# Optimization experiments

Measured on AMD Instinct MI355X. Metric: run time of the kernel, lower is better.

The kernel has to match this reference:

```python
import jax, jax.numpy as jnp
import numpy as np

B, N, C, H, D = 4, 2048, 1024, 16, 64
EPS = 1e-6

def setup_inputs() -> dict:
    key = jax.random.key(0)
    k1, k2, k3 = jax.random.split(key, 3)
    hidden_states = jax.random.normal(k1, (B, N, C), dtype=jnp.float32)
    qkv_w = jax.random.normal(k2, (3 * C, C), dtype=jnp.float32) * (C ** -0.5)
    out_w = jax.random.normal(k3, (C, C), dtype=jnp.float32) * (C ** -0.5)
    norm_q_w = jnp.ones((D,), dtype=jnp.float32)
    norm_k_w = jnp.ones((D,), dtype=jnp.float32)
    # RoPE tables: standard theta=10000 frequencies, rotate-half convention
    inv_freq = 1.0 / (10000.0 ** (jnp.arange(0, D, 2, dtype=jnp.float32) / D))
    pos = jnp.arange(N, dtype=jnp.float32)
    angles = pos[:, None] * inv_freq[None, :]              # [N, D/2]
    angles = jnp.concatenate([angles, angles], axis=-1)    # [N, D]
    cos = jnp.cos(angles)
    sin = jnp.sin(angles)
    return {"hidden_states": hidden_states, "cos": cos, "sin": sin,
            "qkv_w": qkv_w, "out_w": out_w,
            "norm_q_w": norm_q_w, "norm_k_w": norm_k_w}

def _rms_norm(x, w):
    # RMSNorm over last dim (head_dim)
    var = jnp.mean(jnp.square(x), axis=-1, keepdims=True)
    return x * jax.lax.rsqrt(var + EPS) * w

def _rotate_half(x):
    x1, x2 = jnp.split(x, 2, axis=-1)
    return jnp.concatenate([-x2, x1], axis=-1)

def reference(hidden_states, cos, sin, qkv_w, out_w, norm_q_w, norm_k_w):
    # fused QKV projection: [B,N,C] -> [B,N,3,H,D]
    qkv = jnp.einsum('bnc,oc->bno', hidden_states, qkv_w).reshape(B, N, 3, H, D)
    q, k, v = qkv[:, :, 0], qkv[:, :, 1], qkv[:, :, 2]   # each [B,N,H,D]
    q = _rms_norm(q, norm_q_w)
    k = _rms_norm(k, norm_k_w)
    # RoPE, broadcast cos/sin [N,D] -> [1,N,1,D]
    c = cos[None, :, None, :]
    s = sin[None, :, None, :]
    q = q * c + _rotate_half(q) * s
    k = k * c + _rotate_half(k) * s
    # SDPA: softmax(q k^T / sqrt(D)) v, no mask
    scale = D ** -0.5
    scores = jnp.einsum('bqhd,bkhd->bhqk', q, k) * scale   # [B,H,N,N]
    probs = jax.nn.softmax(scores, axis=-1)
    attn = jnp.einsum('bhqk,bkhd->bqhd', probs, v).reshape(B, N, C)
    return jnp.einsum('bnc,oc->bno', attn, out_w)
```

## Files before the change

### kernel.cpp

```cpp
#include <hip/hip_runtime.h>
#include <hip/hip_bf16.h>
#include <math.h>

typedef short bf16x8 __attribute__((ext_vector_type(8)));
typedef float f32x4 __attribute__((ext_vector_type(4)));
typedef float f32x16 __attribute__((ext_vector_type(16)));
typedef __hip_bfloat16 bf16;
typedef unsigned int uint;

static constexpr int Bn = 4, Nn = 2048, Cn = 1024, Hn = 16, Dn = 64;
static constexpr float kEps = 1e-6f;
static constexpr float kQScale = 0.125f * 1.44269504088896340f;

#define GLOAD_LDS16(gp, lp)                                                        \
  __builtin_amdgcn_global_load_lds(                                                \
      (const __attribute__((address_space(1))) unsigned int*)(gp),                 \
      (__attribute__((address_space(3))) unsigned int*)(lp), 16, 0, 0)

__device__ __forceinline__ float exp2_fast(float x) {
#if __has_builtin(__builtin_amdgcn_exp2f)
  return __builtin_amdgcn_exp2f(x);
#else
  return exp2f(x);
#endif
}

__global__ __launch_bounds__(256) void cvt_kernel(const float* __restrict__ in,
                                                  bf16* __restrict__ out, int n4) {
  int i = blockIdx.x * 256 + threadIdx.x;
  if (i >= n4) return;
  const float4 v = reinterpret_cast<const float4*>(in)[i];
  bf16 t[4];
  t[0] = __float2bfloat16(v.x); t[1] = __float2bfloat16(v.y);
  t[2] = __float2bfloat16(v.z); t[3] = __float2bfloat16(v.w);
  reinterpret_cast<uint2*>(out)[i] = *reinterpret_cast<const uint2*>(t);
}

template <int EPI>
__global__ __launch_bounds__(256) void gemm_bt(
    const bf16* __restrict__ A, const bf16* __restrict__ Bw,
    float* __restrict__ Cf, bf16* __restrict__ q_raw, bf16* __restrict__ k_raw,
    bf16* __restrict__ v_buf, const float* __restrict__ cosb,
    const float* __restrict__ sinb, const float* __restrict__ nqw,
    const float* __restrict__ nkw, int nxt, int nyt, int N, int K) {
  __shared__ __align__(16) bf16 As[2][128 * 64];
  __shared__ __align__(16) bf16 Bs[2][128 * 64];
  const int tid = threadIdx.x;
  const int lane = tid & 63, w = tid >> 6;
  const int wr = w >> 1, wc = w & 1;
  const int l15 = lane & 15, l4 = lane >> 4;
  const int bid = blockIdx.x;
  const int xcd = bid & 7;
  const int kk2 = bid >> 3;
  const int nslab = nxt >> 3;
  const int mtile = kk2 / nslab;
  const int ntile = xcd * nslab + (kk2 % nslab);
  const int m0 = mtile * 128, n0 = ntile * 128;
  f32x4 acc[4][4] = {};

  const int sr = tid >> 3, sc = (tid & 7) * 8;
  const int srcE = (((sc * 2) ^ ((sr & 7) << 4)) >> 1);
  const bf16* const Ap = A + (size_t)(m0 + sr) * K + srcE;
  const bf16* const Bp = Bw + (size_t)(n0 + sr) * K + srcE;

#pragma unroll
  for (int c = 0; c < 4; ++c) {
    GLOAD_LDS16(Ap + (size_t)(c * 32) * K, (char*)As[0] + tid * 16 + c * 4096);
    GLOAD_LDS16(Bp + (size_t)(c * 32) * K, (char*)Bs[0] + tid * 16 + c * 4096);
  }
  __syncthreads();

  const int swzg = (l15 & 7) << 4;
  int cur = 0;
  for (int k0 = 0; k0 < K; k0 += 64) {
    if (k0 + 64 < K) {
#pragma unroll
      for (int c = 0; c < 4; ++c) {
        GLOAD_LDS16(Ap + (size_t)(c * 32) * K + k0 + 64,
                    (char*)As[cur ^ 1] + tid * 16 + c * 4096);
        GLOAD_LDS16(Bp + (size_t)(c * 32) * K + k0 + 64,
                    (char*)Bs[cur ^ 1] + tid * 16 + c * 4096);
      }
    }
    const char* Ac = (const char*)As[cur];
    const char* Bc = (const char*)Bs[cur];
#pragma unroll
    for (int kc = 0; kc < 2; ++kc) {
      bf16x8 af[4], bfr[4];
#pragma unroll
      for (int mi = 0; mi < 4; ++mi)
        af[mi] = *reinterpret_cast<const bf16x8*>(
            Ac + (wr * 64 + mi * 16 + l15) * 128 + ((kc * 64 + l4 * 16) ^ swzg));
#pragma unroll
      for (int ni = 0; ni < 4; ++ni)
        bfr[ni] = *reinterpret_cast<const bf16x8*>(
            Bc + (wc * 64 + ni * 16 + l15) * 128 + ((kc * 64 + l4 * 16) ^ swzg));
#pragma unroll
      for (int mi = 0; mi < 4; ++mi)
#pragma unroll
        for (int ni = 0; ni < 4; ++ni)
          acc[mi][ni] =
              __builtin_amdgcn_mfma_f32_16x16x32_bf16(af[mi], bfr[ni], acc[mi][ni], 0, 0, 0);
    }
    __syncthreads();
    cur ^= 1;
  }

  if (EPI == 1) {
#pragma unroll
    for (int mi = 0; mi < 4; ++mi)
#pragma unroll
      for (int ni = 0; ni < 4; ++ni)
#pragma unroll
        for (int r = 0; r < 4; ++r) {
          const int row = m0 + wr * 64 + mi * 16 + l4 * 4 + r;
          const int col = n0 + wc * 64 + ni * 16 + l15;
          Cf[(size_t)row * N + col] = acc[mi][ni][r];
        }
    return;
  }

  const int colbase = n0 + wc * 64;
  const int which = colbase >> 10;
  const int hh = (colbase >> 6) & 15;
  if (which == 2) {
#pragma unroll
    for (int mi = 0; mi < 4; ++mi)
#pragma unroll
      for (int r = 0; r < 4; ++r) {
        const int row = m0 + wr * 64 + mi * 16 + l4 * 4 + r;
        const int b = row >> 11, n = row & (Nn - 1);
#pragma unroll
        for (int ni = 0; ni < 4; ++ni) {
          const int d = ni * 16 + l15;
          const size_t idx = (((size_t)b * Hn + hh) * Nn + n) * Dn + d;
          v_buf[idx] = __float2bfloat16(acc[mi][ni][r]);
        }
      }
    return;
  }
  const float* const wgt = which ? nkw : nqw;
  bf16* const dst = which ? k_raw : q_raw;
  float wv4[4];
#pragma unroll
  for (int ni = 0; ni < 4; ++ni) wv4[ni] = wgt[ni * 16 + l15];
#pragma unroll
  for (int mi = 0; mi < 4; ++mi)
#pragma unroll
    for (int r = 0; r < 4; ++r) {
      const int row = m0 + wr * 64 + mi * 16 + l4 * 4 + r;
      const int b = row >> 11, n = row & (Nn - 1);
      float x0 = acc[mi][0][r], x1 = acc[mi][1][r], x2 = acc[mi][2][r], x3 = acc[mi][3][r];
      float ss = x0 * x0 + x1 * x1 + x2 * x2 + x3 * x3;
      ss += __shfl_xor(ss, 1);
      ss += __shfl_xor(ss, 2);
      ss += __shfl_xor(ss, 4);
      ss += __shfl_xor(ss, 8);
      const float rinv = rsqrtf(ss * (1.f / Dn) + kEps);
      float nx[4] = {x0 * rinv * wv4[0], x1 * rinv * wv4[1], x2 * rinv * wv4[2],
                     x3 * rinv * wv4[3]};
#pragma unroll
      for (int ni = 0; ni < 4; ++ni) {
        const int d = ni * 16 + l15;
        const float c = cosb[n * Dn + d], s = sinb[n * Dn + d];
        const float sgn = (ni < 2) ? -1.f : 1.f;
        float val = nx[ni] * c + sgn * nx[ni ^ 2] * s;
        if (which == 0) val *= kQScale;
        const size_t idx = (((size_t)b * Hn + hh) * Nn + n) * Dn + d;
        dst[idx] = __float2bfloat16(val);
      }
    }
}

__global__ __launch_bounds__(256, 4) void flash_attn(
    const bf16* __restrict__ Qb, const bf16* __restrict__ Kb,
    const bf16* __restrict__ Vb, bf16* __restrict__ Ob) {
  __shared__ __align__(16) char KsB[2][32 * 128];
  __shared__ __align__(16) char VtB[2][64 * 64];
  const int bid = blockIdx.x;
  const int xcd = bid & 7;
  const int kidx = bid >> 3;
  const int bh = xcd * 8 + (kidx >> 4);
  const int q0 = (kidx & 15) * 128;
  const int tid = threadIdx.x, lane = tid & 63, w = tid >> 6;
  const int l31 = lane & 31, hi = lane >> 5;
  const bf16* Qp = Qb + (size_t)bh * Nn * Dn;
  const bf16* Kp = Kb + (size_t)bh * Nn * Dn;
  const bf16* Vp = Vb + (size_t)bh * Nn * Dn;

  const int qrow = q0 + w * 32 + l31;
  bf16x8 qf[4];
#pragma unroll
  for (int dm = 0; dm < 4; ++dm)
    qf[dm] = *reinterpret_cast<const bf16x8*>(&Qp[(size_t)qrow * Dn + dm * 16 + hi * 8]);

  f32x16 Ot0 = {}, Ot1 = {}, Lacc = {};

  const int skk = tid >> 3, sd0 = (tid & 7) * 8;
  const int srcKe = (((sd0 * 2) ^ ((skk & 7) << 4)) >> 1);

  auto stage_v = [&](char* Vn, const uint4& a) {
    const uint wa[4] = {a.x, a.y, a.z, a.w};
#pragma unroll
    for (int j = 0; j < 8; ++j) {
      const int d = sd0 + j;
      const int xs = (((d >> 1) ^ (d >> 3)) & 3) << 4;
      const unsigned short va = (j & 1) ? (unsigned short)(wa[j >> 1] >> 16)
                                        : (unsigned short)(wa[j >> 1] & 0xffff);
      *reinterpret_cast<unsigned short*>(Vn + d * 64 + ((skk * 2) ^ xs)) = va;
    }
  };

  GLOAD_LDS16(Kp + (size_t)skk * Dn + srcKe, KsB[0] + tid * 16);
  {
    uint4 cv = *reinterpret_cast<const uint4*>(&Vp[(size_t)skk * Dn + sd0]);
    stage_v(VtB[0], cv);
  }
  uint4 nv = *reinterpret_cast<const uint4*>(&Vp[(size_t)(32 + skk) * Dn + sd0]);
  __syncthreads();

  const int swzk_rd = (l31 & 7) << 4;
  const int xs0 = ((((l31) >> 1) ^ ((l31) >> 3)) & 3) << 4;
  const int xs1 = ((((32 + l31) >> 1) ^ ((32 + l31) >> 3)) & 3) << 4;
  int cur = 0;
  for (int k0 = 0; k0 < Nn; k0 += 32) {
    const char* Kc = KsB[cur];
    const char* Vc = VtB[cur];

    if (k0 + 32 < Nn) {
      GLOAD_LDS16(Kp + (size_t)(k0 + 32 + skk) * Dn + srcKe, KsB[cur ^ 1] + tid * 16);
      stage_v(VtB[cur ^ 1], nv);
      if (k0 + 64 < Nn)
        nv = *reinterpret_cast<const uint4*>(&Vp[(size_t)(k0 + 64 + skk) * Dn + sd0]);
    }

    f32x16 S0 = {};
    __builtin_amdgcn_s_setprio(1);
#pragma unroll
    for (int dm = 0; dm < 4; ++dm) {
      bf16x8 kf = *reinterpret_cast<const bf16x8*>(
          Kc + l31 * 128 + ((dm * 32 + hi * 16) ^ swzk_rd));
      S0 = __builtin_amdgcn_mfma_f32_32x32x16_bf16(kf, qf[dm], S0, 0, 0, 0);
    }
    __builtin_amdgcn_s_setprio(0);

#pragma unroll
    for (int i = 0; i < 16; ++i) S0[i] = exp2_fast(S0[i]);
#pragma unroll
    for (int i = 0; i < 16; ++i) Lacc[i] += S0[i];
    uint wv[8];
#pragma unroll
    for (int c = 0; c < 2; ++c) {
      uint w0, w1, w2, w3;
      asm("v_cvt_pk_bf16_f32 %0, %1, %2" : "=v"(w0) : "v"(S0[8 * c + 0]), "v"(S0[8 * c + 1]));
      asm("v_cvt_pk_bf16_f32 %0, %1, %2" : "=v"(w1) : "v"(S0[8 * c + 2]), "v"(S0[8 * c + 3]));
      asm("v_cvt_pk_bf16_f32 %0, %1, %2" : "=v"(w2) : "v"(S0[8 * c + 4]), "v"(S0[8 * c + 5]));
      asm("v_cvt_pk_bf16_f32 %0, %1, %2" : "=v"(w3) : "v"(S0[8 * c + 6]), "v"(S0[8 * c + 7]));
      asm("v_permlane32_swap_b32 %0, %1" : "+v"(w0), "+v"(w2));
      asm("v_permlane32_swap_b32 %0, %1" : "+v"(w1), "+v"(w3));
      wv[c * 4 + 0] = w0; wv[c * 4 + 1] = w1;
      wv[c * 4 + 2] = w2; wv[c * 4 + 3] = w3;
    }

    __builtin_amdgcn_s_setprio(1);
#pragma unroll
    for (int s = 0; s < 2; ++s) {
      const uint4 uu = {wv[s * 4 + 0], wv[s * 4 + 1], wv[s * 4 + 2], wv[s * 4 + 3]};
      const bf16x8 pa = __builtin_bit_cast(bf16x8, uu);
      bf16x8 vf0 = *reinterpret_cast<const bf16x8*>(
          Vc + l31 * 64 + ((s * 32 + hi * 16) ^ xs0));
      Ot0 = __builtin_amdgcn_mfma_f32_32x32x16_bf16(vf0, pa, Ot0, 0, 0, 0);
      bf16x8 vf1 = *reinterpret_cast<const bf16x8*>(
          Vc + (32 + l31) * 64 + ((s * 32 + hi * 16) ^ xs1));
      Ot1 = __builtin_amdgcn_mfma_f32_32x32x16_bf16(vf1, pa, Ot1, 0, 0, 0);
    }
    __builtin_amdgcn_s_setprio(0);

    __syncthreads();
    cur ^= 1;
  }

  float l_r = ((Lacc[0] + Lacc[1]) + (Lacc[2] + Lacc[3])) +
              ((Lacc[4] + Lacc[5]) + (Lacc[6] + Lacc[7])) +
              ((Lacc[8] + Lacc[9]) + (Lacc[10] + Lacc[11])) +
              ((Lacc[12] + Lacc[13]) + (Lacc[14] + Lacc[15]));
  l_r += __shfl_xor(l_r, 32);

  const float inv = 1.f / l_r;
  const int b = bh >> 4, h = bh & 15;
#pragma unroll
  for (int dc = 0; dc < 2; ++dc)
#pragma unroll
    for (int a2 = 0; a2 < 4; ++a2) {
      const f32x16& O = dc ? Ot1 : Ot0;
      unsigned short u0 = __bfloat16_as_ushort(__float2bfloat16(O[a2 * 4 + 0] * inv));
      unsigned short u1 = __bfloat16_as_ushort(__float2bfloat16(O[a2 * 4 + 1] * inv));
      unsigned short u2 = __bfloat16_as_ushort(__float2bfloat16(O[a2 * 4 + 2] * inv));
      unsigned short u3 = __bfloat16_as_ushort(__float2bfloat16(O[a2 * 4 + 3] * inv));
      uint2 pk;
      pk.x = (uint)u0 | ((uint)u1 << 16);
      pk.y = (uint)u2 | ((uint)u3 << 16);
      const int col = h * 64 + dc * 32 + a2 * 8 + hi * 4;
      *reinterpret_cast<uint2*>(&Ob[((size_t)(b * Nn + qrow)) * Cn + col]) = pk;
    }
}

extern "C" void kernel_launch(void* const* d_in, const int* in_sizes, int n_in,
                              void* d_out, int out_size, void* d_ws, size_t ws_size,
                              hipStream_t stream) {
  const float* hs   = (const float*)d_in[0];
  const float* cosb = (const float*)d_in[1];
  const float* sinb = (const float*)d_in[2];
  const float* qkvw = (const float*)d_in[3];
  const float* outw = (const float*)d_in[4];
  const float* nqw  = (const float*)d_in[5];
  const float* nkw  = (const float*)d_in[6];
  float* out = (float*)d_out;

  char* ws = (char*)d_ws;
  size_t off = 0;
  bf16* hs_b   = (bf16*)(ws + off); off += (size_t)Bn * Nn * Cn * 2;
  bf16* qkvw_b = (bf16*)(ws + off); off += (size_t)3 * Cn * Cn * 2;
  bf16* outw_b = (bf16*)(ws + off); off += (size_t)Cn * Cn * 2;
  bf16* q_raw  = (bf16*)(ws + off); off += (size_t)Bn * Hn * Nn * Dn * 2;
  bf16* k_raw  = (bf16*)(ws + off); off += (size_t)Bn * Hn * Nn * Dn * 2;
  bf16* v_buf  = (bf16*)(ws + off); off += (size_t)Bn * Hn * Nn * Dn * 2;
  bf16* attn   = (bf16*)(ws + off); off += (size_t)Bn * Nn * Cn * 2;

  cvt_kernel<<<(Bn * Nn * Cn / 4 + 255) / 256, 256, 0, stream>>>(hs, hs_b, Bn * Nn * Cn / 4);
  cvt_kernel<<<(3 * Cn * Cn / 4 + 255) / 256, 256, 0, stream>>>(qkvw, qkvw_b, 3 * Cn * Cn / 4);
  cvt_kernel<<<(Cn * Cn / 4 + 255) / 256, 256, 0, stream>>>(outw, outw_b, Cn * Cn / 4);

  gemm_bt<0><<<24 * 64, 256, 0, stream>>>(
      hs_b, qkvw_b, nullptr, q_raw, k_raw, v_buf, cosb, sinb, nqw, nkw,
      24, 64, 3 * Cn, Cn);

  flash_attn<<<Nn / 128 * Bn * Hn, 256, 0, stream>>>(q_raw, k_raw, v_buf, attn);

  gemm_bt<1><<<8 * 64, 256, 0, stream>>>(
      attn, outw_b, out, nullptr, nullptr, nullptr, nullptr, nullptr, nullptr, nullptr,
      8, 64, Cn, Cn);
}
```

Baseline: 202.9 us.

## Process two K/V tiles per barrier with four-slot LDS ring

The flash attention loop now stages two 32-key K/V tiles per iteration into a four-slot LDS ring and computes both before a single __syncthreads. This halves the number of block barriers and lets global loads for the next pair overlap with two tiles of compute. It doubles LDS use per block, to 32KB, and holds two prefetched V registers, which may reduce occupancy or raise register pressure.

```diff
diff --git a/kernel.cpp b/kernel.cpp
--- a/kernel.cpp
+++ b/kernel.cpp
@@ -175,8 +175,8 @@
 __global__ __launch_bounds__(256, 4) void flash_attn(
     const bf16* __restrict__ Qb, const bf16* __restrict__ Kb,
     const bf16* __restrict__ Vb, bf16* __restrict__ Ob) {
-  __shared__ __align__(16) char KsB[2][32 * 128];
-  __shared__ __align__(16) char VtB[2][64 * 64];
+  __shared__ __align__(16) char KsB[4][32 * 128];
+  __shared__ __align__(16) char VtB[4][64 * 64];
   const int bid = blockIdx.x;
   const int xcd = bid & 7;
   const int kidx = bid >> 3;
@@ -212,72 +212,84 @@
   };
 
   GLOAD_LDS16(Kp + (size_t)skk * Dn + srcKe, KsB[0] + tid * 16);
+  GLOAD_LDS16(Kp + (size_t)(32 + skk) * Dn + srcKe, KsB[1] + tid * 16);
   {
-    uint4 cv = *reinterpret_cast<const uint4*>(&Vp[(size_t)skk * Dn + sd0]);
-    stage_v(VtB[0], cv);
-  }
-  uint4 nv = *reinterpret_cast<const uint4*>(&Vp[(size_t)(32 + skk) * Dn + sd0]);
+    uint4 cv0 = *reinterpret_cast<const uint4*>(&Vp[(size_t)skk * Dn + sd0]);
+    uint4 cv1 = *reinterpret_cast<const uint4*>(&Vp[(size_t)(32 + skk) * Dn + sd0]);
+    stage_v(VtB[0], cv0);
+    stage_v(VtB[1], cv1);
+  }
+  uint4 nva = *reinterpret_cast<const uint4*>(&Vp[(size_t)(64 + skk) * Dn + sd0]);
+  uint4 nvb = *reinterpret_cast<const uint4*>(&Vp[(size_t)(96 + skk) * Dn + sd0]);
   __syncthreads();
 
   const int swzk_rd = (l31 & 7) << 4;
   const int xs0 = ((((l31) >> 1) ^ ((l31) >> 3)) & 3) << 4;
   const int xs1 = ((((32 + l31) >> 1) ^ ((32 + l31) >> 3)) & 3) << 4;
-  int cur = 0;
-  for (int k0 = 0; k0 < Nn; k0 += 32) {
-    const char* Kc = KsB[cur];
-    const char* Vc = VtB[cur];
-
-    if (k0 + 32 < Nn) {
-      GLOAD_LDS16(Kp + (size_t)(k0 + 32 + skk) * Dn + srcKe, KsB[cur ^ 1] + tid * 16);
-      stage_v(VtB[cur ^ 1], nv);
-      if (k0 + 64 < Nn)
-        nv = *reinterpret_cast<const uint4*>(&Vp[(size_t)(k0 + 64 + skk) * Dn + sd0]);
-    }
-
-    f32x16 S0 = {};
-    __builtin_amdgcn_s_setprio(1);
-#pragma unroll
-    for (int dm = 0; dm < 4; ++dm) {
-      bf16x8 kf = *reinterpret_cast<const bf16x8*>(
-          Kc + l31 * 128 + ((dm * 32 + hi * 16) ^ swzk_rd));
-      S0 = __builtin_amdgcn_mfma_f32_32x32x16_bf16(kf, qf[dm], S0, 0, 0, 0);
-    }
-    __builtin_amdgcn_s_setprio(0);
-
-#pragma unroll
-    for (int i = 0; i < 16; ++i) S0[i] = exp2_fast(S0[i]);
-#pragma unroll
-    for (int i = 0; i < 16; ++i) Lacc[i] += S0[i];
-    uint wv[8];
-#pragma unroll
-    for (int c = 0; c < 2; ++c) {
-      uint w0, w1, w2, w3;
-      asm("v_cvt_pk_bf16_f32 %0, %1, %2" : "=v"(w0) : "v"(S0[8 * c + 0]), "v"(S0[8 * c + 1]));
-      asm("v_cvt_pk_bf16_f32 %0, %1, %2" : "=v"(w1) : "v"(S0[8 * c + 2]), "v"(S0[8 * c + 3]));
-      asm("v_cvt_pk_bf16_f32 %0, %1, %2" : "=v"(w2) : "v"(S0[8 * c + 4]), "v"(S0[8 * c + 5]));
-      asm("v_cvt_pk_bf16_f32 %0, %1, %2" : "=v"(w3) : "v"(S0[8 * c + 6]), "v"(S0[8 * c + 7]));
-      asm("v_permlane32_swap_b32 %0, %1" : "+v"(w0), "+v"(w2));
-      asm("v_permlane32_swap_b32 %0, %1" : "+v"(w1), "+v"(w3));
-      wv[c * 4 + 0] = w0; wv[c * 4 + 1] = w1;
-      wv[c * 4 + 2] = w2; wv[c * 4 + 3] = w3;
-    }
-
-    __builtin_amdgcn_s_setprio(1);
-#pragma unroll
-    for (int s = 0; s < 2; ++s) {
-      const uint4 uu = {wv[s * 4 + 0], wv[s * 4 + 1], wv[s * 4 + 2], wv[s * 4 + 3]};
-      const bf16x8 pa = __builtin_bit_cast(bf16x8, uu);
-      bf16x8 vf0 = *reinterpret_cast<const bf16x8*>(
-          Vc + l31 * 64 + ((s * 32 + hi * 16) ^ xs0));
-      Ot0 = __builtin_amdgcn_mfma_f32_32x32x16_bf16(vf0, pa, Ot0, 0, 0, 0);
-      bf16x8 vf1 = *reinterpret_cast<const bf16x8*>(
-          Vc + (32 + l31) * 64 + ((s * 32 + hi * 16) ^ xs1));
-      Ot1 = __builtin_amdgcn_mfma_f32_32x32x16_bf16(vf1, pa, Ot1, 0, 0, 0);
-    }
-    __builtin_amdgcn_s_setprio(0);
+
+  for (int t = 0; t < 64; t += 2) {
+    if (t + 2 < 64) {
+      GLOAD_LDS16(Kp + (size_t)((t + 2) * 32 + skk) * Dn + srcKe,
+                  KsB[(t + 2) & 3] + tid * 16);
+      GLOAD_LDS16(Kp + (size_t)((t + 3) * 32 + skk) * Dn + srcKe,
+                  KsB[(t + 3) & 3] + tid * 16);
+      stage_v(VtB[(t + 2) & 3], nva);
+      stage_v(VtB[(t + 3) & 3], nvb);
+      if (t + 4 < 64) {
+        nva = *reinterpret_cast<const uint4*>(&Vp[(size_t)((t + 4) * 32 + skk) * Dn + sd0]);
+        nvb = *reinterpret_cast<const uint4*>(&Vp[(size_t)((t + 5) * 32 + skk) * Dn + sd0]);
+      }
+    }
+
+#pragma unroll
+    for (int u = 0; u < 2; ++u) {
+      const char* Kc = KsB[(t + u) & 3];
+      const char* Vc = VtB[(t + u) & 3];
+
+      f32x16 S0 = {};
+      __builtin_amdgcn_s_setprio(1);
+#pragma unroll
+      for (int dm = 0; dm < 4; ++dm) {
+        bf16x8 kf = *reinterpret_cast<const bf16x8*>(
+            Kc + l31 * 128 + ((dm * 32 + hi * 16) ^ swzk_rd));
+        S0 = __builtin_amdgcn_mfma_f32_32x32x16_bf16(kf, qf[dm], S0, 0, 0, 0);
+      }
+      __builtin_amdgcn_s_setprio(0);
+
+#pragma unroll
+      for (int i = 0; i < 16; ++i) S0[i] = exp2_fast(S0[i]);
+#pragma unroll
+      for (int i = 0; i < 16; ++i) Lacc[i] += S0[i];
+      uint wv[8];
+#pragma unroll
+      for (int c = 0; c < 2; ++c) {
+        uint w0, w1, w2, w3;
+        asm("v_cvt_pk_bf16_f32 %0, %1, %2" : "=v"(w0) : "v"(S0[8 * c + 0]), "v"(S0[8 * c + 1]));
+        asm("v_cvt_pk_bf16_f32 %0, %1, %2" : "=v"(w1) : "v"(S0[8 * c + 2]), "v"(S0[8 * c + 3]));
+        asm("v_cvt_pk_bf16_f32 %0, %1, %2" : "=v"(w2) : "v"(S0[8 * c + 4]), "v"(S0[8 * c + 5]));
+        asm("v_cvt_pk_bf16_f32 %0, %1, %2" : "=v"(w3) : "v"(S0[8 * c + 6]), "v"(S0[8 * c + 7]));
+        asm("v_permlane32_swap_b32 %0, %1" : "+v"(w0), "+v"(w2));
+        asm("v_permlane32_swap_b32 %0, %1" : "+v"(w1), "+v"(w3));
+        wv[c * 4 + 0] = w0; wv[c * 4 + 1] = w1;
+        wv[c * 4 + 2] = w2; wv[c * 4 + 3] = w3;
+      }
+
+      __builtin_amdgcn_s_setprio(1);
+#pragma unroll
+      for (int s = 0; s < 2; ++s) {
+        const uint4 uu = {wv[s * 4 + 0], wv[s * 4 + 1], wv[s * 4 + 2], wv[s * 4 + 3]};
+        const bf16x8 pa = __builtin_bit_cast(bf16x8, uu);
+        bf16x8 vf0 = *reinterpret_cast<const bf16x8*>(
+            Vc + l31 * 64 + ((s * 32 + hi * 16) ^ xs0));
+        Ot0 = __builtin_amdgcn_mfma_f32_32x32x16_bf16(vf0, pa, Ot0, 0, 0, 0);
+        bf16x8 vf1 = *reinterpret_cast<const bf16x8*>(
+            Vc + (32 + l31) * 64 + ((s * 32 + hi * 16) ^ xs1));
+        Ot1 = __builtin_amdgcn_mfma_f32_32x32x16_bf16(vf1, pa, Ot1, 0, 0, 0);
+      }
+      __builtin_amdgcn_s_setprio(0);
+    }
 
     __syncthreads();
-    cur ^= 1;
   }
 
   float l_r = ((Lacc[0] + Lacc[1]) + (Lacc[2] + Lacc[3])) +
```

Measured after the change: 204.2 us. Within noise of the previous version (+0.6%).
